# Optimization experiments

Measured on AMD Instinct MI355X. Metric: run time of the kernel, lower is better.

## Reference

```python
import jax, jax.numpy as jnp
import numpy as np

D_MODEL = 1024
N_HEAD = 16
T = 2048
HEAD = D_MODEL // N_HEAD  # 64
RANKS = [32, 16, 8, 8]
BLOCKS = [2048, 1024, 512, 256]  # seq_len // 2**i ('default')
OFFS = np.cumsum([0] + RANKS)


def setup_inputs() -> dict:
    key = jax.random.key(0)
    k0, k1, k2 = jax.random.split(key, 3)
    s = 0.02
    x = jax.random.normal(k0, (1, T, D_MODEL), dtype=jnp.float32)
    W_attn = jax.random.normal(k1, (D_MODEL, 3 * D_MODEL), dtype=jnp.float32) * s
    b_attn = jnp.zeros((3 * D_MODEL,), dtype=jnp.float32)
    W_proj = jax.random.normal(k2, (D_MODEL, D_MODEL), dtype=jnp.float32) * s
    b_proj = jnp.zeros((D_MODEL,), dtype=jnp.float32)
    return {"x": x, "W_attn": W_attn, "b_attn": b_attn, "W_proj": W_proj, "b_proj": b_proj}


def reference(x, W_attn, b_attn, W_proj, b_proj):
    B = x.shape[0]
    qkv = x @ W_attn + b_attn  # (B,T,3*D)
    q, k, v = jnp.split(qkv, 3, axis=-1)
    # (B,H,T,HEAD)
    q = q.reshape(B, T, N_HEAD, HEAD).transpose(0, 2, 1, 3)
    k = k.reshape(B, T, N_HEAD, HEAD).transpose(0, 2, 1, 3)
    v = v.reshape(B, T, N_HEAD, HEAD).transpose(0, 2, 1, 3)

    att = jnp.zeros((B, N_HEAD, T, T), dtype=x.dtype)
    for i, (bdx, r) in enumerate(zip(BLOCKS, RANKS)):
        nb = T // bdx
        qi = q[..., OFFS[i]:OFFS[i + 1]].reshape(B, N_HEAD, nb, bdx, r)
        ki = k[..., OFFS[i]:OFFS[i + 1]].reshape(B, N_HEAD, nb, bdx, r)
        blk = jnp.einsum('bhnir,bhnjr->bhnij', qi, ki) * (1.0 / r)  # (B,H,nb,bdx,bdx)
        # scatter block-diagonal scores into full T x T matrix
        att5 = att.reshape(B, N_HEAD, nb, bdx, nb, bdx)
        ar = jnp.arange(nb)
        att5 = att5.at[:, :, ar, :, ar, :].add(jnp.moveaxis(blk, 2, 0))
        att = att5.reshape(B, N_HEAD, T, T)

    causal = jnp.tril(jnp.ones((T, T), dtype=bool))
    att = jnp.where(causal, att, -jnp.inf)
    att = jax.nn.softmax(att, axis=-1)
    y = att @ v  # (B,H,T,HEAD)
    y = y.transpose(0, 2, 1, 3).reshape(B, T, D_MODEL)
    return y @ W_proj + b_proj
```

## Files before the change

kernel.cpp:

```cpp
#include <hip/hip_runtime.h>

using bf16x8 = __attribute__((ext_vector_type(8))) short;
using u16x8  = __attribute__((ext_vector_type(8))) unsigned short;
using f32x4  = __attribute__((ext_vector_type(4))) float;

#define DEVI __device__ __forceinline__

#define LOG2E 1.4426950408889634f

DEVI unsigned short f2bf(float f) {
  union { float ff; unsigned u; } v; v.ff = f;
  unsigned r = v.u + 0x7FFFu + ((v.u >> 16) & 1u);
  return (unsigned short)(r >> 16);
}

DEVI float bf2f(unsigned short s) {
  union { unsigned u; float f; } t; t.u = ((unsigned)s) << 16;
  return t.f;
}

DEVI int cvtpk(float lo, float hi) {
  int r;
  asm("v_cvt_pk_bf16_f32 %0, %1, %2" : "=v"(r) : "v"(lo), "v"(hi));
  return r;
}

DEVI void g2l16(const void* g, void* l) {
  __builtin_amdgcn_global_load_lds(
      (const __attribute__((address_space(1))) unsigned int*)g,
      (__attribute__((address_space(3))) unsigned int*)l, 16, 0, 0);
}

__global__ __launch_bounds__(256) void k_prep(
    const float* __restrict__ x, const float* __restrict__ Wa, const float* __restrict__ Wp,
    unsigned short* __restrict__ xb, unsigned short* __restrict__ WaT,
    unsigned short* __restrict__ WpT) {
  __shared__ unsigned short tile[32][33];
  const int b = blockIdx.x;
  const int tid = threadIdx.x;
  if (b < 2048) {
    const int i = b * 256 + tid;
    float4 v = reinterpret_cast<const float4*>(x)[i];
    ushort4 o;
    o.x = f2bf(v.x); o.y = f2bf(v.y); o.z = f2bf(v.z); o.w = f2bf(v.w);
    reinterpret_cast<ushort4*>(xb)[i] = o;
    return;
  }
  const float* in;
  unsigned short* out;
  int c0, r0, C;
  if (b < 5120) {
    const int bb = b - 2048;
    in = Wa; out = WaT; C = 3072;
    c0 = (bb % 96) * 32; r0 = (bb / 96) * 32;
  } else {
    const int bb = b - 5120;
    in = Wp; out = WpT; C = 1024;
    c0 = (bb & 31) * 32; r0 = (bb >> 5) * 32;
  }
  const int xx = tid & 31, yy = tid >> 5;
  for (int i = yy; i < 32; i += 8) tile[i][xx] = f2bf(in[(size_t)(r0 + i) * C + c0 + xx]);
  __syncthreads();
  for (int i = yy; i < 32; i += 8) out[(size_t)(c0 + i) * 1024 + r0 + xx] = tile[xx][i];
}

__global__ __launch_bounds__(256) void k_gemm_qkv(
    const unsigned short* __restrict__ A, const unsigned short* __restrict__ Bt,
    const float* __restrict__ bias,
    unsigned short* __restrict__ qs, unsigned short* __restrict__ kbuf,
    unsigned short* __restrict__ vT) {
  constexpr int K = 1024;
  __shared__ __align__(16) unsigned short As[2][128 * 64];
  __shared__ __align__(16) unsigned short Bs[2][64 * 64];
  const int lane = threadIdx.x & 63, wid = threadIdx.x >> 6;
  const int bx = blockIdx.x;
  const int nt = (bx & 7) * 6 + (bx >> 3);
  const int m0 = blockIdx.y * 128, n0 = nt * 64;
  const int wr = (wid >> 1) * 64, wc = (wid & 1) * 32;
  const int g = lane >> 4, li = lane & 15;
  f32x4 acc[4][2] = {};

#define STAGE_QKV(buf, k0)                                                              \
  {                                                                                     \
    _Pragma("unroll")                                                                   \
    for (int c = wid * 4; c < wid * 4 + 4; c++) {                                       \
      const int flat = c * 1024 + lane * 16;                                            \
      const int row = flat >> 7, colb = flat & 127;                                     \
      g2l16((const char*)A + ((size_t)(m0 + row) * K + (k0)) * 2 + colb,                \
            (char*)As[buf] + c * 1024);                                                 \
    }                                                                                   \
    _Pragma("unroll")                                                                   \
    for (int c = wid * 2; c < wid * 2 + 2; c++) {                                       \
      const int flat = c * 1024 + lane * 16;                                            \
      const int row = flat >> 7, colb = flat & 127;                                     \
      g2l16((const char*)Bt + ((size_t)(n0 + row) * K + (k0)) * 2 + colb,               \
            (char*)Bs[buf] + c * 1024);                                                 \
    }                                                                                   \
  }

  STAGE_QKV(0, 0);
  __syncthreads();
  int buf = 0;
  for (int t = 0; t < 16; t++) {
    if (t < 15) STAGE_QKV(buf ^ 1, (t + 1) * 64);
#pragma unroll
    for (int ks = 0; ks < 2; ks++) {
      const int kk = ks * 32 + g * 8;
      bf16x8 a[4], b[2];
#pragma unroll
      for (int i = 0; i < 4; i++)
        a[i] = *reinterpret_cast<const bf16x8*>(As[buf] + (wr + i * 16 + li) * 64 + kk);
#pragma unroll
      for (int j = 0; j < 2; j++)
        b[j] = *reinterpret_cast<const bf16x8*>(Bs[buf] + (wc + j * 16 + li) * 64 + kk);
#pragma unroll
      for (int i = 0; i < 4; i++)
#pragma unroll
        for (int j = 0; j < 2; j++)
          acc[i][j] = __builtin_amdgcn_mfma_f32_16x16x32_bf16(a[i], b[j], acc[i][j], 0, 0, 0);
    }
    __syncthreads();
    buf ^= 1;
  }

  const int rb = m0 + wr + g * 4;
  const int cb = n0 + wc + li;
  const int region = n0 >> 10;
  if (region == 0) {
#pragma unroll
    for (int j = 0; j < 2; j++) {
      const int c = cb + j * 16;
      const float bv = bias[c];
      const int hq = c >> 6, d = c & 63;
      const float sc = (d < 32 ? 0.03125f : (d < 48 ? 0.0625f : 0.125f)) * LOG2E;
#pragma unroll
      for (int i = 0; i < 4; i++)
#pragma unroll
        for (int r = 0; r < 4; r++)
          qs[((size_t)(hq * 2048 + rb + i * 16 + r) << 6) + d] = f2bf((acc[i][j][r] + bv) * sc);
    }
  } else if (region == 1) {
#pragma unroll
    for (int j = 0; j < 2; j++) {
      const int c = cb + j * 16;
      const float bv = bias[c];
      const int hq = (c >> 6) - 16, d = c & 63;
#pragma unroll
      for (int i = 0; i < 4; i++)
#pragma unroll
        for (int r = 0; r < 4; r++)
          kbuf[((size_t)(hq * 2048 + rb + i * 16 + r) << 6) + d] = f2bf(acc[i][j][r] + bv);
    }
  } else {
#pragma unroll
    for (int j = 0; j < 2; j++) {
      const int c = cb + j * 16;
      const float bv = bias[c];
      const int row = c - 2048;
#pragma unroll
      for (int i = 0; i < 4; i++) {
        const int t0 = rb + i * 16;
        ushort4 pk;
        pk.x = f2bf(acc[i][j][0] + bv);
        pk.y = f2bf(acc[i][j][1] + bv);
        pk.z = f2bf(acc[i][j][2] + bv);
        pk.w = f2bf(acc[i][j][3] + bv);
        *reinterpret_cast<ushort4*>(vT + (size_t)row * 2048 + t0) = pk;
      }
    }
  }
#undef STAGE_QKV
}

DEVI int chunk_off(int qt) {
  const int off[17] = {0,1,2,4,6,9,12,16,20,25,30,36,42,49,56,64,72};
  return off[qt];
}

__global__ __launch_bounds__(256) void k_attn_part(
    const unsigned short* __restrict__ qs, const unsigned short* __restrict__ kbuf,
    const unsigned short* __restrict__ vT,
    unsigned short* __restrict__ o_part, float* __restrict__ ml,
    unsigned short* __restrict__ yb) {
  __shared__ __align__(16) unsigned short Ks[2][128 * 64];
  __shared__ __align__(16) unsigned short Vs[2][64 * 128];
  const int lane = threadIdx.x & 63, wid = threadIdx.x >> 6;
  const int g = lane >> 4, li = lane & 15;

  const int h = blockIdx.x / 72;
  const int rem = blockIdx.x % 72;
  int qt = 0;
#pragma unroll
  for (int i = 0; i < 16; i++)
    if (rem >= chunk_off(i + 1)) qt = i + 1;
  const int ci = rem - chunk_off(qt);
  const int kt0 = ci * 2;
  const int kt1 = min(qt, kt0 + 1);
  const int q0 = qt * 128;

  const bf16x8 bzero = {0, 0, 0, 0, 0, 0, 0, 0};

#define STAGE_KV(buf, kt)                                                               \
  for (int c = wid; c < 16; c += 4) {                                                   \
    const int fb = c * 1024;                                                            \
    const int flat = fb + lane * 16;                                                    \
    {                                                                                   \
      const int row = flat >> 7;                                                        \
      const int cs = (((flat >> 4) & 7) ^ (row & 7)) << 4;                              \
      g2l16((const char*)kbuf + (((size_t)(h * 2048 + (kt) * 128 + row)) << 7) + cs,    \
            (char*)Ks[buf] + fb);                                                       \
    }                                                                                   \
    {                                                                                   \
      const int row = flat >> 8;                                                        \
      const int cs = (((flat >> 4) & 15) ^ (row & 15)) << 4;                            \
      g2l16((const char*)vT + ((size_t)(h * 64 + row) * 2048 + (kt) * 128) * 2 + cs,    \
            (char*)Vs[buf] + fb);                                                       \
    }                                                                                   \
  }

  STAGE_KV(0, kt0);
  if (kt1 > kt0) STAGE_KV(1, kt0 + 1);

  bf16x8 qf[2][2];
#pragma unroll
  for (int mi = 0; mi < 2; mi++)
#pragma unroll
    for (int ks = 0; ks < 2; ks++) {
      const int t = q0 + wid * 32 + mi * 16 + li;
      const int d = ks * 32 + g * 8;
      qf[mi][ks] = *reinterpret_cast<const bf16x8*>(qs + ((size_t)(h * 2048 + t) << 6) + d);
    }

  f32x4 o[2][4] = {};
  float m_run[2] = {-1e30f, -1e30f}, l_run[2] = {0.f, 0.f};

  const int q256 = qt >> 1;
  __syncthreads();

  int buf = 0;
  for (int kt = kt0; kt <= kt1; kt++) {
    const int x = q256 ^ (kt >> 1);
    const int Keff = (x == 0) ? 64 : ((x >= 4) ? 32 : ((x >= 2) ? 48 : 56));

    f32x4 st[8][2] = {};
    __builtin_amdgcn_s_setprio(1);
#pragma unroll
    for (int cf = 0; cf < 8; cf++) {
      const int krow = cf * 16 + li;
      const bf16x8 a0 = *reinterpret_cast<const bf16x8*>(
          Ks[buf] + krow * 64 + ((g ^ (krow & 7)) << 3));
      st[cf][0] = __builtin_amdgcn_mfma_f32_16x16x32_bf16(a0, qf[0][0], st[cf][0], 0, 0, 0);
      st[cf][1] = __builtin_amdgcn_mfma_f32_16x16x32_bf16(a0, qf[1][0], st[cf][1], 0, 0, 0);
    }
    if (Keff > 32) {
      const bool zf = (32 + g * 8) >= Keff;
#pragma unroll
      for (int cf = 0; cf < 8; cf++) {
        const int krow = cf * 16 + li;
        bf16x8 a1 = *reinterpret_cast<const bf16x8*>(
            Ks[buf] + krow * 64 + (((4 + g) ^ (krow & 7)) << 3));
        if (zf) a1 = bzero;
        st[cf][0] = __builtin_amdgcn_mfma_f32_16x16x32_bf16(a1, qf[0][1], st[cf][0], 0, 0, 0);
        st[cf][1] = __builtin_amdgcn_mfma_f32_16x16x32_bf16(a1, qf[1][1], st[cf][1], 0, 0, 0);
      }
    }
    __builtin_amdgcn_s_setprio(0);

    if (kt == qt) {
#pragma unroll
      for (int cf = 0; cf < 8; cf++)
#pragma unroll
        for (int mi = 0; mi < 2; mi++)
#pragma unroll
          for (int r = 0; r < 4; r++) {
            const int t2 = cf * 16 + g * 4 + r;
            const int qq = wid * 32 + mi * 16 + li;
            if (t2 > qq) st[cf][mi][r] = -1e30f;
          }
    }

    int pk[2][8][2];
#pragma unroll
    for (int mi = 0; mi < 2; mi++) {
      float c4[8];
#pragma unroll
      for (int cf = 0; cf < 8; cf++)
        c4[cf] = fmaxf(fmaxf(st[cf][mi][0], st[cf][mi][1]),
                       fmaxf(st[cf][mi][2], st[cf][mi][3]));
      const float ta = fmaxf(fmaxf(c4[0], c4[1]), fmaxf(c4[2], c4[3]));
      const float tb = fmaxf(fmaxf(c4[4], c4[5]), fmaxf(c4[6], c4[7]));
      float tm = fmaxf(ta, tb);
      tm = fmaxf(tm, __shfl_xor(tm, 16));
      tm = fmaxf(tm, __shfl_xor(tm, 32));
      if (!__all(tm <= m_run[mi] + 12.0f)) {
        const float mn = fmaxf(m_run[mi], tm);
        const float corr = exp2f(m_run[mi] - mn);
        m_run[mi] = mn;
        l_run[mi] *= corr;
        float cb0 = __shfl(corr, 4 * g + 0);
        float cb1 = __shfl(corr, 4 * g + 1);
        float cb2 = __shfl(corr, 4 * g + 2);
        float cb3 = __shfl(corr, 4 * g + 3);
#pragma unroll
        for (int nf = 0; nf < 4; nf++) {
          o[mi][nf][0] *= cb0; o[mi][nf][1] *= cb1;
          o[mi][nf][2] *= cb2; o[mi][nf][3] *= cb3;
        }
      }
      const float mn = m_run[mi];
      float sum = 0.f;
#pragma unroll
      for (int cf = 0; cf < 8; cf++) {
        const float p0 = exp2f(st[cf][mi][0] - mn);
        const float p1 = exp2f(st[cf][mi][1] - mn);
        const float p2 = exp2f(st[cf][mi][2] - mn);
        const float p3 = exp2f(st[cf][mi][3] - mn);
        sum += (p0 + p1) + (p2 + p3);
        pk[mi][cf][0] = cvtpk(p0, p1);
        pk[mi][cf][1] = cvtpk(p2, p3);
      }
      sum += __shfl_xor(sum, 16);
      sum += __shfl_xor(sum, 32);
      l_run[mi] += sum;
    }

    __builtin_amdgcn_s_setprio(1);
#pragma unroll
    for (int ks2 = 0; ks2 < 4; ks2++) {
      bf16x8 pa[2];
#pragma unroll
      for (int mi = 0; mi < 2; mi++) {
        union { int i[4]; bf16x8 v; } u;
        u.i[0] = pk[mi][2 * ks2][0];
        u.i[1] = pk[mi][2 * ks2][1];
        u.i[2] = pk[mi][2 * ks2 + 1][0];
        u.i[3] = pk[mi][2 * ks2 + 1][1];
        pa[mi] = u.v;
      }
      bf16x8 vb[4];
#pragma unroll
      for (int nf = 0; nf < 4; nf++) {
        const int vrow = nf * 16 + li;
        const int rm = vrow & 15;
        const int ch0 = 4 * ks2 + (g >> 1);
        const int b8 = (g & 1) * 8;
        union { struct { int2 lo, hi; } p; bf16x8 v; } u;
        u.p.lo = *reinterpret_cast<const int2*>(
            (const char*)Vs[buf] + vrow * 256 + (((ch0 + 0) ^ rm) << 4) + b8);
        u.p.hi = *reinterpret_cast<const int2*>(
            (const char*)Vs[buf] + vrow * 256 + (((ch0 + 2) ^ rm) << 4) + b8);
        vb[nf] = u.v;
      }
#pragma unroll
      for (int mi = 0; mi < 2; mi++)
#pragma unroll
        for (int nf = 0; nf < 4; nf++)
          o[mi][nf] = __builtin_amdgcn_mfma_f32_16x16x32_bf16(pa[mi], vb[nf], o[mi][nf], 0, 0, 0);
    }
    __builtin_amdgcn_s_setprio(0);
    buf ^= 1;
  }
#undef STAGE_KV

  if (qt < 2) {
#pragma unroll
    for (int mi = 0; mi < 2; mi++) {
      const float inv = 1.0f / l_run[mi];
      float ib[4];
      ib[0] = __shfl(inv, 4 * g + 0);
      ib[1] = __shfl(inv, 4 * g + 1);
      ib[2] = __shfl(inv, 4 * g + 2);
      ib[3] = __shfl(inv, 4 * g + 3);
#pragma unroll
      for (int nf = 0; nf < 4; nf++)
#pragma unroll
        for (int r = 0; r < 4; r++) {
          const int t = q0 + wid * 32 + mi * 16 + g * 4 + r;
          yb[(size_t)t * 1024 + h * 64 + nf * 16 + li] = f2bf(o[mi][nf][r] * ib[r]);
        }
    }
    return;
  }

  const size_t pbase = (size_t)blockIdx.x * 8192;
#pragma unroll
  for (int mi = 0; mi < 2; mi++) {
#pragma unroll
    for (int nf = 0; nf < 4; nf++)
#pragma unroll
      for (int r = 0; r < 4; r++) {
        const int row = wid * 32 + mi * 16 + g * 4 + r;
        o_part[pbase + (size_t)row * 64 + nf * 16 + li] = f2bf(o[mi][nf][r]);
      }
  }
  if (g == 0) {
#pragma unroll
    for (int mi = 0; mi < 2; mi++) {
      const int row = wid * 32 + mi * 16 + li;
      ml[(size_t)blockIdx.x * 256 + row] = m_run[mi];
      ml[(size_t)blockIdx.x * 256 + 128 + row] = l_run[mi];
    }
  }
}

__global__ __launch_bounds__(256) void k_combine(
    const unsigned short* __restrict__ o_part, const float* __restrict__ ml,
    unsigned short* __restrict__ yb) {
  const int h = blockIdx.x / 14, qt = blockIdx.x % 14 + 2;
  const int nc = (qt >> 1) + 1;
  const int base = h * 72 + chunk_off(qt);
  const int row = threadIdx.x >> 1;
  const int c0 = (threadIdx.x & 1) * 32;

  float M = -1e30f;
  for (int ci = 0; ci < nc; ci++)
    M = fmaxf(M, ml[(size_t)(base + ci) * 256 + row]);
  float L = 0.f;
  for (int ci = 0; ci < nc; ci++) {
    const float m = ml[(size_t)(base + ci) * 256 + row];
    const float l = ml[(size_t)(base + ci) * 256 + 128 + row];
    L += exp2f(m - M) * l;
  }
  const float inv = 1.0f / L;

  float acc[32];
#pragma unroll
  for (int j = 0; j < 32; j++) acc[j] = 0.f;
  for (int ci = 0; ci < nc; ci++) {
    const float wc = exp2f(ml[(size_t)(base + ci) * 256 + row] - M);
    const u16x8* src = reinterpret_cast<const u16x8*>(
        o_part + (size_t)(base + ci) * 8192 + (size_t)row * 64 + c0);
#pragma unroll
    for (int j8 = 0; j8 < 4; j8++) {
      u16x8 v = src[j8];
#pragma unroll
      for (int e = 0; e < 8; e++) acc[j8 * 8 + e] += wc * bf2f(v[e]);
    }
  }
  const int t = qt * 128 + row;
  unsigned short* dst = yb + (size_t)t * 1024 + h * 64 + c0;
#pragma unroll
  for (int j8 = 0; j8 < 4; j8++) {
    ushort4 pk;
    pk.x = f2bf(acc[j8 * 8 + 0] * inv);
    pk.y = f2bf(acc[j8 * 8 + 1] * inv);
    pk.z = f2bf(acc[j8 * 8 + 2] * inv);
    pk.w = f2bf(acc[j8 * 8 + 3] * inv);
    ushort4 pk2;
    pk2.x = f2bf(acc[j8 * 8 + 4] * inv);
    pk2.y = f2bf(acc[j8 * 8 + 5] * inv);
    pk2.z = f2bf(acc[j8 * 8 + 6] * inv);
    pk2.w = f2bf(acc[j8 * 8 + 7] * inv);
    reinterpret_cast<ushort4*>(dst)[j8 * 2 + 0] = pk;
    reinterpret_cast<ushort4*>(dst)[j8 * 2 + 1] = pk2;
  }
}

__global__ __launch_bounds__(256) void k_gemm_proj(
    const unsigned short* __restrict__ A, const unsigned short* __restrict__ Bt,
    const float* __restrict__ bias, float* __restrict__ out) {
  constexpr int K = 1024;
  __shared__ __align__(16) unsigned short As[2][64 * 64];
  __shared__ __align__(16) unsigned short Bs[2][64 * 64];
  const int lane = threadIdx.x & 63, wid = threadIdx.x >> 6;
  const int bx = blockIdx.x;
  const int nt = (bx & 7) * 2 + (bx >> 3);
  const int m0 = blockIdx.y * 64, n0 = nt * 64;
  const int wr = (wid >> 1) * 32, wc = (wid & 1) * 32;
  const int g = lane >> 4, li = lane & 15;
  f32x4 acc[2][2] = {};

#define STAGE_PROJ(buf, k0)                                                             \
  {                                                                                     \
    _Pragma("unroll")                                                                   \
    for (int c = wid * 2; c < wid * 2 + 2; c++) {                                       \
      const int flat = c * 1024 + lane * 16;                                            \
      const int row = flat >> 7, colb = flat & 127;                                     \
      g2l16((const char*)A + ((size_t)(m0 + row) * K + (k0)) * 2 + colb,                \
            (char*)As[buf] + c * 1024);                                                 \
      g2l16((const char*)Bt + ((size_t)(n0 + row) * K + (k0)) * 2 + colb,               \
            (char*)Bs[buf] + c * 1024);                                                 \
    }                                                                                   \
  }

  STAGE_PROJ(0, 0);
  __syncthreads();
  int buf = 0;
  for (int t = 0; t < 16; t++) {
    if (t < 15) STAGE_PROJ(buf ^ 1, (t + 1) * 64);
#pragma unroll
    for (int ks = 0; ks < 2; ks++) {
      const int kk = ks * 32 + g * 8;
      bf16x8 a[2], b[2];
#pragma unroll
      for (int i = 0; i < 2; i++)
        a[i] = *reinterpret_cast<const bf16x8*>(As[buf] + (wr + i * 16 + li) * 64 + kk);
#pragma unroll
      for (int j = 0; j < 2; j++)
        b[j] = *reinterpret_cast<const bf16x8*>(Bs[buf] + (wc + j * 16 + li) * 64 + kk);
#pragma unroll
      for (int i = 0; i < 2; i++)
#pragma unroll
        for (int j = 0; j < 2; j++)
          acc[i][j] = __builtin_amdgcn_mfma_f32_16x16x32_bf16(a[i], b[j], acc[i][j], 0, 0, 0);
    }
    __syncthreads();
    buf ^= 1;
  }

  const int rb = m0 + wr + g * 4;
  const int cb = n0 + wc + li;
#pragma unroll
  for (int j = 0; j < 2; j++) {
    const int c = cb + j * 16;
    const float bv = bias[c];
#pragma unroll
    for (int i = 0; i < 2; i++) {
#pragma unroll
      for (int r = 0; r < 4; r++) {
        const int t = rb + i * 16 + r;
        out[(size_t)t * 1024 + c] = acc[i][j][r] + bv;
      }
    }
  }
#undef STAGE_PROJ
}

extern "C" void kernel_launch(void* const* d_in, const int* in_sizes, int n_in,
                              void* d_out, int out_size, void* d_ws, size_t ws_size,
                              hipStream_t stream) {
  const float* x      = (const float*)d_in[0];
  const float* W_attn = (const float*)d_in[1];
  const float* b_attn = (const float*)d_in[2];
  const float* W_proj = (const float*)d_in[3];
  const float* b_proj = (const float*)d_in[4];
  float* out = (float*)d_out;
  char* ws = (char*)d_ws;
  const size_t MB = 1024 * 1024;
  unsigned short* xb  = (unsigned short*)(ws + 0 * MB);
  unsigned short* WaT = (unsigned short*)(ws + 4 * MB);
  unsigned short* WpT = (unsigned short*)(ws + 10 * MB);
  unsigned short* qs  = (unsigned short*)(ws + 12 * MB);
  unsigned short* kb  = (unsigned short*)(ws + 16 * MB);
  unsigned short* vT  = (unsigned short*)(ws + 20 * MB);
  unsigned short* yb  = (unsigned short*)(ws + 24 * MB);
  unsigned short* o_part = (unsigned short*)(ws + 28 * MB);
  float* ml     = (float*)(ws + 48 * MB);

  k_prep<<<dim3(6144), dim3(256), 0, stream>>>(x, W_attn, W_proj, xb, WaT, WpT);
  k_gemm_qkv<<<dim3(48, 16), dim3(256), 0, stream>>>(xb, WaT, b_attn, qs, kb, vT);
  k_attn_part<<<dim3(1152), dim3(256), 0, stream>>>(qs, kb, vT, o_part, ml, yb);
  k_combine<<<dim3(224), dim3(256), 0, stream>>>(o_part, ml, yb);
  k_gemm_proj<<<dim3(16, 32), dim3(256), 0, stream>>>(yb, WpT, b_proj, out);
}
```

Measured before the change: 97.00 us.

## Fuse split-KV combine into attention kernel via last-block atomic counter

Removes the separate combine kernel. Each attention partial block now publishes its output and m/l stats, fences, and atomically bumps a per-(head, query tile) counter. The last block to arrive performs the log-sum-exp merge and writes the final bf16 rows. This saves one kernel launch and the tail gap between kernels, at the cost of atomics, fences and some serialized combine work done by the last blocks. The counters are reset in the prep kernel.

After: 353.6 us. 265% more time.

```diff
diff --git a/kernel.cpp b/kernel.cpp
--- a/kernel.cpp
+++ b/kernel.cpp
@@ -5,7 +5,6 @@
 using f32x4  = __attribute__((ext_vector_type(4))) float;
 
 #define DEVI __device__ __forceinline__
-
 #define LOG2E 1.4426950408889634f
 
 DEVI unsigned short f2bf(float f) {
@@ -34,11 +33,12 @@
 __global__ __launch_bounds__(256) void k_prep(
     const float* __restrict__ x, const float* __restrict__ Wa, const float* __restrict__ Wp,
     unsigned short* __restrict__ xb, unsigned short* __restrict__ WaT,
-    unsigned short* __restrict__ WpT) {
+    unsigned short* __restrict__ WpT, int* __restrict__ cnt) {
   __shared__ unsigned short tile[32][33];
   const int b = blockIdx.x;
   const int tid = threadIdx.x;
   if (b < 2048) {
+    if (b == 0) cnt[tid] = 0;
     const int i = b * 256 + tid;
     float4 v = reinterpret_cast<const float4*>(x)[i];
     ushort4 o;
@@ -181,9 +181,10 @@
     const unsigned short* __restrict__ qs, const unsigned short* __restrict__ kbuf,
     const unsigned short* __restrict__ vT,
     unsigned short* __restrict__ o_part, float* __restrict__ ml,
-    unsigned short* __restrict__ yb) {
+    unsigned short* __restrict__ yb, int* __restrict__ cnt) {
   __shared__ __align__(16) unsigned short Ks[2][128 * 64];
   __shared__ __align__(16) unsigned short Vs[2][64 * 128];
+  __shared__ int last_flag;
   const int lane = threadIdx.x & 63, wid = threadIdx.x >> 6;
   const int g = lane >> 4, li = lane & 15;
 
@@ -197,7 +198,6 @@
   const int kt0 = ci * 2;
   const int kt1 = min(qt, kt0 + 1);
   const int q0 = qt * 128;
-
   const bf16x8 bzero = {0, 0, 0, 0, 0, 0, 0, 0};
 
 #define STAGE_KV(buf, kt)                                                               \
@@ -233,14 +233,13 @@
 
   f32x4 o[2][4] = {};
   float m_run[2] = {-1e30f, -1e30f}, l_run[2] = {0.f, 0.f};
-
   const int q256 = qt >> 1;
   __syncthreads();
 
   int buf = 0;
   for (int kt = kt0; kt <= kt1; kt++) {
-    const int x = q256 ^ (kt >> 1);
-    const int Keff = (x == 0) ? 64 : ((x >= 4) ? 32 : ((x >= 2) ? 48 : 56));
+    const int xx = q256 ^ (kt >> 1);
+    const int Keff = (xx == 0) ? 64 : ((xx >= 4) ? 32 : ((xx >= 2) ? 48 : 56));
 
     f32x4 st[8][2] = {};
     __builtin_amdgcn_s_setprio(1);
@@ -384,7 +383,7 @@
 
   const size_t pbase = (size_t)blockIdx.x * 8192;
 #pragma unroll
-  for (int mi = 0; mi < 2; mi++) {
+  for (int mi = 0; mi < 2; mi++)
 #pragma unroll
     for (int nf = 0; nf < 4; nf++)
 #pragma unroll
@@ -392,7 +391,6 @@
         const int row = wid * 32 + mi * 16 + g * 4 + r;
         o_part[pbase + (size_t)row * 64 + nf * 16 + li] = f2bf(o[mi][nf][r]);
       }
-  }
   if (g == 0) {
 #pragma unroll
     for (int mi = 0; mi < 2; mi++) {
@@ -401,24 +399,27 @@
       ml[(size_t)blockIdx.x * 256 + 128 + row] = l_run[mi];
     }
   }
-}
-
-__global__ __launch_bounds__(256) void k_combine(
-    const unsigned short* __restrict__ o_part, const float* __restrict__ ml,
-    unsigned short* __restrict__ yb) {
-  const int h = blockIdx.x / 14, qt = blockIdx.x % 14 + 2;
+
+  __threadfence();
+  __syncthreads();
   const int nc = (qt >> 1) + 1;
+  if (threadIdx.x == 0)
+    last_flag = (atomicAdd(&cnt[h * 16 + qt], 1) == nc - 1);
+  __syncthreads();
+  if (!last_flag) return;
+  __threadfence();
+
   const int base = h * 72 + chunk_off(qt);
   const int row = threadIdx.x >> 1;
   const int c0 = (threadIdx.x & 1) * 32;
 
   float M = -1e30f;
-  for (int ci = 0; ci < nc; ci++)
-    M = fmaxf(M, ml[(size_t)(base + ci) * 256 + row]);
+  for (int c2 = 0; c2 < nc; c2++)
+    M = fmaxf(M, ml[(size_t)(base + c2) * 256 + row]);
   float L = 0.f;
-  for (int ci = 0; ci < nc; ci++) {
-    const float m = ml[(size_t)(base + ci) * 256 + row];
-    const float l = ml[(size_t)(base + ci) * 256 + 128 + row];
+  for (int c2 = 0; c2 < nc; c2++) {
+    const float m = ml[(size_t)(base + c2) * 256 + row];
+    const float l = ml[(size_t)(base + c2) * 256 + 128 + row];
     L += exp2f(m - M) * l;
   }
   const float inv = 1.0f / L;
@@ -426,10 +427,10 @@
   float acc[32];
 #pragma unroll
   for (int j = 0; j < 32; j++) acc[j] = 0.f;
-  for (int ci = 0; ci < nc; ci++) {
-    const float wc = exp2f(ml[(size_t)(base + ci) * 256 + row] - M);
+  for (int c2 = 0; c2 < nc; c2++) {
+    const float wc = exp2f(ml[(size_t)(base + c2) * 256 + row] - M);
     const u16x8* src = reinterpret_cast<const u16x8*>(
-        o_part + (size_t)(base + ci) * 8192 + (size_t)row * 64 + c0);
+        o_part + (size_t)(base + c2) * 8192 + (size_t)row * 64 + c0);
 #pragma unroll
     for (int j8 = 0; j8 < 4; j8++) {
       u16x8 v = src[j8];
@@ -546,10 +547,10 @@
   unsigned short* yb  = (unsigned short*)(ws + 24 * MB);
   unsigned short* o_part = (unsigned short*)(ws + 28 * MB);
   float* ml     = (float*)(ws + 48 * MB);
-
-  k_prep<<<dim3(6144), dim3(256), 0, stream>>>(x, W_attn, W_proj, xb, WaT, WpT);
+  int* cnt      = (int*)(ws + 50 * MB);
+
+  k_prep<<<dim3(6144), dim3(256), 0, stream>>>(x, W_attn, W_proj, xb, WaT, WpT, cnt);
   k_gemm_qkv<<<dim3(48, 16), dim3(256), 0, stream>>>(xb, WaT, b_attn, qs, kb, vT);
-  k_attn_part<<<dim3(1152), dim3(256), 0, stream>>>(qs, kb, vT, o_part, ml, yb);
-  k_combine<<<dim3(224), dim3(256), 0, stream>>>(o_part, ml, yb);
+  k_attn_part<<<dim3(1152), dim3(256), 0, stream>>>(qs, kb, vT, o_part, ml, yb, cnt);
   k_gemm_proj<<<dim3(16, 32), dim3(256), 0, stream>>>(yb, WpT, b_proj, out);
 }
```
